# Kernel optimization log

Hardware: AMD Instinct MI355X
Metric: run time of the kernel (lower is better)

Reference implementation:

```python
import jax, jax.numpy as jnp
import numpy as np

N_NODES = 50000
N_EDGES = 800000
N_GRAPHS = 256
DROPOUT = 0.3


def _dropout(x, key, rate=DROPOUT):
    keep = 1.0 - rate
    mask = jax.random.bernoulli(key, keep, x.shape)
    return jnp.where(mask, x / keep, 0.0).astype(x.dtype)


def _gcn_conv(x, W, b, src, dst, num_nodes):
    # PyG GCNConv: symmetric norm with self-loops, edge_weight = 1.
    # deg over destination (col) including self-loop.
    deg = jnp.zeros((num_nodes,), x.dtype).at[dst].add(1.0) + 1.0
    dinv = jax.lax.rsqrt(deg)                       # [N]
    h = x @ W                                       # [N, F] GEMM first (F small)
    norm = dinv[src] * dinv[dst]                    # [E]
    msg = h[src] * norm[:, None]                    # [E, F] gather + scale
    agg = jnp.zeros_like(h).at[dst].add(msg)        # scatter-add
    agg = agg + h * (dinv * dinv)[:, None]          # self-loop contribution
    return agg + b


def setup_inputs() -> dict:
    key = jax.random.key(0)
    ks = jax.random.split(key, 8)
    d_in, d_h, d_out = 64, 64, 10
    s = lambda k, sh, fan: jax.random.normal(k, sh, jnp.float32) / np.sqrt(fan)
    return {
        "x": jax.random.normal(ks[0], (N_NODES, d_in), jnp.float32),
        "edge_index": jax.random.randint(ks[1], (2, N_EDGES), 0, N_NODES, jnp.int64),
        "batch": jnp.sort(jax.random.randint(ks[2], (N_NODES,), 0, N_GRAPHS, jnp.int64)),
        "W1": s(ks[3], (d_in, d_h), d_in), "b1": jnp.zeros((d_h,), jnp.float32),
        "W2": s(ks[4], (d_h, d_h), d_h),   "b2": jnp.zeros((d_h,), jnp.float32),
        "W3": s(ks[5], (d_h, d_h), d_h),   "b3": jnp.zeros((d_h,), jnp.float32),
        "Wl": s(ks[6], (d_h, d_out), d_h), "bl": jnp.zeros((d_out,), jnp.float32),
    }


def reference(x, edge_index, batch, W1, b1, W2, b2, W3, b3, Wl, bl):
    src, dst = edge_index[0], edge_index[1]
    dk = jax.random.split(jax.random.key(12345), 3)

    h = _gcn_conv(x, W1, b1, src, dst, N_NODES)
    h = _dropout(jax.nn.relu(h), dk[0])
    h = _gcn_conv(h, W2, b2, src, dst, N_NODES)
    h = _dropout(jax.nn.relu(h), dk[1])
    h = _gcn_conv(h, W3, b3, src, dst, N_NODES)

    # global mean pool over graphs
    sums = jax.ops.segment_sum(h, batch, num_segments=N_GRAPHS)          # [G, F]
    cnts = jax.ops.segment_sum(jnp.ones((h.shape[0],), h.dtype), batch,
                               num_segments=N_GRAPHS)                    # [G]
    pooled = sums / jnp.maximum(cnts, 1.0)[:, None]

    pooled = _dropout(pooled, dk[2])
    return pooled @ Wl + bl
```

## Files before the change

### kernel.cpp

```cpp
#include <hip/hip_runtime.h>

typedef unsigned int u32;
typedef unsigned short u16;
using bfrag  = __attribute__((ext_vector_type(8))) short;
using f32x4  = __attribute__((ext_vector_type(4))) float;

#define CHUNK 4096
#define KPT 16
#define NBUCK 128
#define BCAP 10496
#define CSRCAP (BCAP + 4096)

__host__ __device__ inline void tf2x32(u32 k0, u32 k1, u32 x0, u32 x1,
                                       u32* y0, u32* y1) {
    u32 ks2 = k0 ^ k1 ^ 0x1BD11BDAu;
#define TFR(r) { x0 += x1; x1 = (x1 << (r)) | (x1 >> (32 - (r))); x1 ^= x0; }
    x0 += k0; x1 += k1;
    TFR(13) TFR(15) TFR(26) TFR(6)
    x0 += k1;  x1 += ks2 + 1u;
    TFR(17) TFR(29) TFR(16) TFR(24)
    x0 += ks2; x1 += k0 + 2u;
    TFR(13) TFR(15) TFR(26) TFR(6)
    x0 += k0;  x1 += k1 + 3u;
    TFR(17) TFR(29) TFR(16) TFR(24)
    x0 += k1;  x1 += ks2 + 4u;
    TFR(13) TFR(15) TFR(26) TFR(6)
    x0 += ks2; x1 += k0 + 5u;
#undef TFR
    *y0 = x0; *y1 = x1;
}

__device__ inline float drop_scale(float v, u32 k0, u32 k1, u32 idx) {
    u32 y0, y1;
    tf2x32(k0, k1, 0u, idx, &y0, &y1);
    u32 bits = y0 ^ y1;
    float u = __uint_as_float((bits >> 9) | 0x3f800000u) - 1.0f;
    return (u < 0.7f) ? (v / 0.7f) : 0.0f;
}

__device__ inline u16 f2bf(float f) {
    u32 u = __float_as_uint(f);
    u32 r = (u + 0x7fffu + ((u >> 16) & 1u)) >> 16;
    return (u16)r;
}
__device__ inline float bf2f(u16 h) { return __uint_as_float(((u32)h) << 16); }

__device__ inline int idx_at(const void* p, long i, int is64) {
    return is64 ? (int)((const long long*)p)[i] : ((const int*)p)[i];
}

__global__ void k_init(const u32* p, int* flag, int* gCur1,
                       const float* __restrict__ W0, const float* __restrict__ W1,
                       const float* __restrict__ W2, u16* __restrict__ wsw,
                       float* __restrict__ sums, int ZN, u16* __restrict__ Hb, int N) {
    if (blockIdx.x == 0) {
        int tid = threadIdx.x;
        if (tid < NBUCK) gCur1[tid] = tid * BCAP;
        if (tid < 64) Hb[((long)N << 6) + tid] = 0;
        for (int i = tid; i < ZN; i += 256) sums[i] = 0.0f;
        if (tid == 0) {
            int all0 = 1;
            for (int i = 0; i < 64; ++i)
                if (p[2 * i + 1] != 0u) { all0 = 0; break; }
            *flag = all0;
        }
        return;
    }
    int t = (blockIdx.x - 1) * 256 + threadIdx.x;
    if (t >= 3 * 4096) return;
    int layer = t >> 12, r = t & 4095;
    int nt = r >> 10, ks = (r >> 9) & 1, lane = (r >> 3) & 63, j = r & 7;
    const float* W = (layer == 0) ? W0 : ((layer == 1) ? W1 : W2);
    int k = ks * 32 + (lane >> 4) * 8 + j;
    int n = nt * 16 + (lane & 15);
    wsw[t] = f2bf(W[k * 64 + n]);
}

__global__ __launch_bounds__(256) void k_binscat(
    const void* ei, int E, const int* flag,
    int* __restrict__ gCur1, u32* __restrict__ binned) {
    __shared__ u32 stage[CHUNK];
    __shared__ int cnt[NBUCK], offsx[NBUCK], cur[NBUCK], gbase[NBUCK], scn[NBUCK];
    int tid = threadIdx.x;
    long base = (long)blockIdx.x * CHUNK;
    int is64 = *flag;
    if (tid < NBUCK) { cnt[tid] = 0; cur[tid] = 0; }
    __syncthreads();
    u32 rec[KPT];
#pragma unroll
    for (int k = 0; k < KPT; ++k) {
        long e = base + k * 256 + tid;
        u32 r = 0xFFFFFFFFu;
        if (e < E) {
            int s = idx_at(ei, e, is64);
            int d = idx_at(ei, (long)E + e, is64);
            r = ((u32)d << 16) | (u32)s;
            atomicAdd(&cnt[d >> 9], 1);
        }
        rec[k] = r;
    }
    __syncthreads();
    if (tid < NBUCK) scn[tid] = cnt[tid];
    __syncthreads();
    for (int d = 1; d < NBUCK; d <<= 1) {
        int t2 = 0;
        if (tid < NBUCK && tid >= d) t2 = scn[tid - d];
        __syncthreads();
        if (tid < NBUCK) scn[tid] += t2;
        __syncthreads();
    }
    if (tid < NBUCK) offsx[tid] = scn[tid] - cnt[tid];
    __syncthreads();
#pragma unroll
    for (int k = 0; k < KPT; ++k) {
        u32 r = rec[k];
        if (r != 0xFFFFFFFFu) {
            int bk = r >> 25;
            int p = offsx[bk] + atomicAdd(&cur[bk], 1);
            stage[p] = r;
        }
    }
    __syncthreads();
    if (tid < NBUCK && cnt[tid] > 0)
        gbase[tid] = atomicAdd(&gCur1[tid], cnt[tid]);
    __syncthreads();
    int total = scn[NBUCK - 1];
    for (int i = tid; i < total; i += 256) {
        u32 r = stage[i];
        int bk = r >> 25;
        binned[gbase[bk] + (i - offsx[bk])] = r;
    }
}

__global__ __launch_bounds__(512) void k_csrfill(
    const u32* __restrict__ binned, const int* __restrict__ gCur1,
    int* __restrict__ offs, int* __restrict__ degi, float* __restrict__ dinv,
    u16* __restrict__ csr, int N) {
    __shared__ int lcnt[512];
    __shared__ int lcur[512];
    int b = blockIdx.x;
    int n0 = b << 9;
    int nn = N - n0; if (nn > 512) nn = 512;
    int tid = threadIdx.x;
    lcnt[tid] = 0;
    __syncthreads();
    int rbeg = b * BCAP, rend = gCur1[b];
    for (int i = rbeg + tid; i < rend; i += 512)
        atomicAdd(&lcnt[(int)(binned[i] >> 16) - n0], 1);
    __syncthreads();
    int v = lcnt[tid];
    int pv = (v + 7) & ~7;
    __syncthreads();
    lcnt[tid] = pv;
    __syncthreads();
    for (int d = 1; d < 512; d <<= 1) {
        int t2 = (tid >= d) ? lcnt[tid - d] : 0;
        __syncthreads();
        lcnt[tid] += t2;
        __syncthreads();
    }
    int pexcl = lcnt[tid] - pv;
    int o = b * CSRCAP + pexcl;
    if (tid < nn) {
        offs[n0 + tid] = o;
        degi[n0 + tid] = v;
        dinv[n0 + tid] = rsqrtf((float)v + 1.0f);
        lcur[tid] = o;
        for (int i = v; i < pv; ++i) csr[o + i] = (u16)N;
    }
    __syncthreads();
    for (int i = rbeg + tid; i < rend; i += 512) {
        u32 r = binned[i];
        int pos = atomicAdd(&lcur[(int)(r >> 16) - n0], 1);
        csr[pos] = (u16)(r & 0xFFFFu);
    }
}

__global__ __launch_bounds__(256) void k_gemm_mfma(
    const u16* __restrict__ Ab, const float* __restrict__ Af,
    const u16* __restrict__ Wsw, const float* __restrict__ dinv,
    u16* __restrict__ Hout, int N, int use_f32) {
    int wid = blockIdx.x * 4 + (threadIdx.x >> 6);
    int lane = threadIdx.x & 63;
    int row0 = wid * 16;
    if (row0 >= N) return;
    int rl = lane & 15, kg = lane >> 4;
    int arow = row0 + rl; if (arow >= N) arow = N - 1;
    bfrag a0, a1;
    if (use_f32) {
        const float* r = Af + (long)arow * 64 + kg * 8;
        float4 v0 = *(const float4*)(r);
        float4 v1 = *(const float4*)(r + 4);
        float4 v2 = *(const float4*)(r + 32);
        float4 v3 = *(const float4*)(r + 36);
        a0[0] = (short)f2bf(v0.x); a0[1] = (short)f2bf(v0.y);
        a0[2] = (short)f2bf(v0.z); a0[3] = (short)f2bf(v0.w);
        a0[4] = (short)f2bf(v1.x); a0[5] = (short)f2bf(v1.y);
        a0[6] = (short)f2bf(v1.z); a0[7] = (short)f2bf(v1.w);
        a1[0] = (short)f2bf(v2.x); a1[1] = (short)f2bf(v2.y);
        a1[2] = (short)f2bf(v2.z); a1[3] = (short)f2bf(v2.w);
        a1[4] = (short)f2bf(v3.x); a1[5] = (short)f2bf(v3.y);
        a1[6] = (short)f2bf(v3.z); a1[7] = (short)f2bf(v3.w);
    } else {
        a0 = *(const bfrag*)(Ab + (long)arow * 64 + kg * 8);
        a1 = *(const bfrag*)(Ab + (long)arow * 64 + 32 + kg * 8);
    }
    float d4[4];
#pragma unroll
    for (int i = 0; i < 4; ++i) {
        int row = row0 + kg * 4 + i;
        d4[i] = (row < N) ? dinv[row] : 0.0f;
    }
#pragma unroll
    for (int nt = 0; nt < 4; ++nt) {
        bfrag b0 = *(const bfrag*)(Wsw + ((nt * 2 + 0) * 64 + lane) * 8);
        bfrag b1 = *(const bfrag*)(Wsw + ((nt * 2 + 1) * 64 + lane) * 8);
        f32x4 acc = {0.0f, 0.0f, 0.0f, 0.0f};
        acc = __builtin_amdgcn_mfma_f32_16x16x32_bf16(a0, b0, acc, 0, 0, 0);
        acc = __builtin_amdgcn_mfma_f32_16x16x32_bf16(a1, b1, acc, 0, 0, 0);
        int col = nt * 16 + rl;
#pragma unroll
        for (int i = 0; i < 4; ++i) {
            int row = row0 + kg * 4 + i;
            if (row < N) Hout[(long)row * 64 + col] = f2bf(d4[i] * acc[i]);
        }
    }
}

__global__ __launch_bounds__(256) void k_agg(
    const u16* __restrict__ csr, const int* __restrict__ offs,
    const int* __restrict__ degi, const float* __restrict__ dinv,
    const u16* __restrict__ Hb, const float* __restrict__ b,
    u16* __restrict__ Gb, int N, int mode, u32 k0, u32 k1) {
    long t = (long)blockIdx.x * blockDim.x + threadIdx.x;
    int node = (int)(t >> 4);
    int q = (int)(t & 15);
    if (node >= N) return;
    int beg = offs[node];
    int deg = degi[node];
    int pv = (deg + 7) & ~7;
    float a0 = 0.0f, a1 = 0.0f, a2 = 0.0f, a3 = 0.0f;
    const u16* cp = csr + beg;
    ushort4 cA, cB;
    if (pv > 0) {
        cA = *(const ushort4*)cp;
        cB = *(const ushort4*)(cp + 4);
    }
    for (int g = 0; g < pv; g += 8) {
        ushort4 nA = *(const ushort4*)(cp + g + 8);
        ushort4 nB = *(const ushort4*)(cp + g + 12);
        u16 ids[8] = {cA.x, cA.y, cA.z, cA.w, cB.x, cB.y, cB.z, cB.w};
#pragma unroll
        for (int u = 0; u < 8; ++u) {
            uint2 d = *(const uint2*)(Hb + ((long)ids[u] << 6) + (q << 2));
            a0 += __uint_as_float(d.x << 16);
            a1 += __uint_as_float(d.x & 0xffff0000u);
            a2 += __uint_as_float(d.y << 16);
            a3 += __uint_as_float(d.y & 0xffff0000u);
        }
        cA = nA; cB = nB;
    }
    float di = dinv[node];
    uint2 hd = *(const uint2*)(Hb + ((long)node << 6) + (q << 2));
    float4 bv = *(const float4*)(b + (q << 2));
    float v0 = di * (a0 + __uint_as_float(hd.x << 16))         + bv.x;
    float v1 = di * (a1 + __uint_as_float(hd.x & 0xffff0000u)) + bv.y;
    float v2 = di * (a2 + __uint_as_float(hd.y << 16))         + bv.z;
    float v3 = di * (a3 + __uint_as_float(hd.y & 0xffff0000u)) + bv.w;
    u32 idx = ((u32)node << 6) + (q << 2);
    if (mode) {
        v0 = drop_scale(fmaxf(v0, 0.0f), k0, k1, idx + 0);
        v1 = drop_scale(fmaxf(v1, 0.0f), k0, k1, idx + 1);
        v2 = drop_scale(fmaxf(v2, 0.0f), k0, k1, idx + 2);
        v3 = drop_scale(fmaxf(v3, 0.0f), k0, k1, idx + 3);
    }
    ushort4 o; o.x = f2bf(v0); o.y = f2bf(v1); o.z = f2bf(v2); o.w = f2bf(v3);
    *(ushort4*)(Gb + idx) = o;
}

__global__ void k_poolsum(const u16* __restrict__ Gb, const void* batch,
                          const int* flag, int N,
                          float* __restrict__ sums, float* __restrict__ cnt) {
    int wave = (int)(((long)blockIdx.x * blockDim.x + threadIdx.x) >> 6);
    int f = threadIdx.x & 63;
    int n0 = wave * 8;
    if (n0 >= N) return;
    int nend = n0 + 8 < N ? n0 + 8 : N;
    int is64 = *flag;
    float acc = 0.0f; float cacc = 0.0f; int curg = -1;
    for (int n = n0; n < nend; ++n) {
        int g = idx_at(batch, n, is64);
        if (g != curg) {
            if (curg >= 0) {
                atomicAdd(&sums[curg * 64 + f], acc);
                if (f == 0) atomicAdd(&cnt[curg], cacc);
            }
            curg = g; acc = 0.0f; cacc = 0.0f;
        }
        acc += bf2f(Gb[(long)n * 64 + f]);
        cacc += 1.0f;
    }
    if (curg >= 0) {
        atomicAdd(&sums[curg * 64 + f], acc);
        if (f == 0) atomicAdd(&cnt[curg], cacc);
    }
}

__global__ void k_poolout(const float* __restrict__ sums, const float* __restrict__ cnt,
                          const float* __restrict__ Wl, const float* __restrict__ bl,
                          float* __restrict__ out, u32 k0, u32 k1, int O) {
    __shared__ float p_sh[64];
    int g = blockIdx.x;
    int t = threadIdx.x;
    float c = fmaxf(cnt[g], 1.0f);
    float pv = drop_scale(sums[g * 64 + t] / c, k0, k1, (u32)(g * 64 + t));
    p_sh[t] = pv;
    __syncthreads();
    if (t < O) {
        float acc = bl[t];
#pragma unroll 8
        for (int k = 0; k < 64; ++k) acc += p_sh[k] * Wl[k * O + t];
        out[g * O + t] = acc;
    }
}

extern "C" void kernel_launch(void* const* d_in, const int* in_sizes, int n_in,
                              void* d_out, int out_size, void* d_ws, size_t ws_size,
                              hipStream_t stream) {
    const float* x  = (const float*)d_in[0];
    const void*  ei = d_in[1];
    const void*  bt = d_in[2];
    const float* W[3] = {(const float*)d_in[3], (const float*)d_in[5], (const float*)d_in[7]};
    const float* b[3] = {(const float*)d_in[4], (const float*)d_in[6], (const float*)d_in[8]};
    const float* Wl = (const float*)d_in[9];
    const float* bl = (const float*)d_in[10];
    float* out = (float*)d_out;

    const int F = 64;
    int N  = in_sizes[0] / F;
    int E  = in_sizes[1] / 2;
    int NG = 256;
    int O  = in_sizes[9] / F;
    long NF = (long)N * F;
    int Np = ((N + 63) / 64) * 64;
    int NB = (N + 511) >> 9;

    auto align256 = [](char*& p) { p = (char*)(((size_t)p + 255) & ~(size_t)255); };
    char* wp = (char*)d_ws;
    align256(wp); float* dinv   = (float*)wp;  wp += (size_t)Np * 4;
    align256(wp); int*   degi   = (int*)wp;    wp += (size_t)Np * 4;
    align256(wp); int*   offs   = (int*)wp;    wp += (size_t)Np * 4;
    align256(wp); int*   flag   = (int*)wp;    wp += 256;
    align256(wp); int*   gCur1  = (int*)wp;    wp += NBUCK * 4;
    align256(wp); float* sums   = (float*)wp;  wp += (size_t)NG * F * 4;
    align256(wp); float* cnt    = (float*)wp;  wp += (size_t)NG * 4;
    align256(wp); u16*   wsw    = (u16*)wp;    wp += 3 * 4096 * 2;
    align256(wp); u32*   binned = (u32*)wp;    wp += (size_t)NBUCK * BCAP * 4;
    align256(wp); u16*   csr    = (u16*)wp;    wp += (size_t)NBUCK * CSRCAP * 2;
    align256(wp); u16*   Hb     = (u16*)wp;    wp += NF * 2 + 128;
    align256(wp); u16*   Gb     = (u16*)wp;    wp += NF * 2;

    u32 dk[3][2];
    for (u32 i = 0; i < 3; ++i) tf2x32(0u, 12345u, 0u, i, &dk[i][0], &dk[i][1]);

    int EB = (E + CHUNK - 1) / CHUNK;
    int ZN = NG * F + NG;

    k_init<<<49, 256, 0, stream>>>((const u32*)ei, flag, gCur1,
                                   W[0], W[1], W[2], wsw, sums, ZN, Hb, N);
    k_binscat<<<EB, 256, 0, stream>>>(ei, E, flag, gCur1, binned);
    k_csrfill<<<NB, 512, 0, stream>>>(binned, gCur1, offs, degi, dinv, csr, N);

    int gemmBlocks = ((N + 15) / 16 + 3) / 4;
    int aggBlocks = (int)(((long)N * 16 + 255) / 256);
    for (int l = 0; l < 3; ++l) {
        k_gemm_mfma<<<gemmBlocks, 256, 0, stream>>>(Gb, x, wsw + l * 4096, dinv,
                                                    Hb, N, (l == 0) ? 1 : 0);
        k_agg<<<aggBlocks, 256, 0, stream>>>(csr, offs, degi, dinv, Hb, b[l],
                                             Gb, N, (l < 2) ? 1 : 0,
                                             dk[l][0], dk[l][1]);
    }

    int pw = (N + 7) / 8;
    k_poolsum<<<(int)(((long)pw * 64 + 255) / 256), 256, 0, stream>>>(Gb, bt, flag, N, sums, cnt);
    k_poolout<<<NG, 64, 0, stream>>>(sums, cnt, Wl, bl, out, dk[2][0], dk[2][1], O);
}
```

Baseline: 137.7 us.

## Fuse next-layer GEMM into aggregation and simplify edge binning with fixed slots

Layers 1 and 2 now run one kernel that aggregates neighbours, applies bias, ReLU and dropout, stages the 16-node tile in shared memory, and multiplies by the next weight matrix with MFMA. This removes two GEMM launches and the round trip of the intermediate activation through global memory. Edge binning drops the per-block prefix scan in favour of fixed 72-slot shared buckets, with overflow going to a small list or to direct global atomics. The catch is that each aggregation block now also holds the GEMM work, and skewed buckets can push extra traffic onto global atomics.

```diff
diff --git a/kernel.cpp b/kernel.cpp
--- a/kernel.cpp
+++ b/kernel.cpp
@@ -8,6 +8,7 @@
 #define CHUNK 4096
 #define KPT 16
 #define NBUCK 128
+#define SCAP 72
 #define BCAP 10496
 #define CSRCAP (BCAP + 4096)
 
@@ -52,11 +53,15 @@
 __global__ void k_init(const u32* p, int* flag, int* gCur1,
                        const float* __restrict__ W0, const float* __restrict__ W1,
                        const float* __restrict__ W2, u16* __restrict__ wsw,
-                       float* __restrict__ sums, int ZN, u16* __restrict__ Hb, int N) {
+                       float* __restrict__ sums, int ZN,
+                       u16* __restrict__ HbA, u16* __restrict__ HbB, int N) {
     if (blockIdx.x == 0) {
         int tid = threadIdx.x;
         if (tid < NBUCK) gCur1[tid] = tid * BCAP;
-        if (tid < 64) Hb[((long)N << 6) + tid] = 0;
+        if (tid < 64) {
+            HbA[((long)N << 6) + tid] = 0;
+            HbB[((long)N << 6) + tid] = 0;
+        }
         for (int i = tid; i < ZN; i += 256) sums[i] = 0.0f;
         if (tid == 0) {
             int all0 = 1;
@@ -79,56 +84,51 @@
 __global__ __launch_bounds__(256) void k_binscat(
     const void* ei, int E, const int* flag,
     int* __restrict__ gCur1, u32* __restrict__ binned) {
-    __shared__ u32 stage[CHUNK];
-    __shared__ int cnt[NBUCK], offsx[NBUCK], cur[NBUCK], gbase[NBUCK], scn[NBUCK];
+    __shared__ u32 stage[NBUCK * SCAP];
+    __shared__ int cnt[NBUCK], gbase[NBUCK];
+    __shared__ u32 olist[256];
+    __shared__ int ocnt;
     int tid = threadIdx.x;
+    if (tid < NBUCK) cnt[tid] = 0;
+    if (tid == 0) ocnt = 0;
+    __syncthreads();
+    int is64 = *flag;
     long base = (long)blockIdx.x * CHUNK;
-    int is64 = *flag;
-    if (tid < NBUCK) { cnt[tid] = 0; cur[tid] = 0; }
-    __syncthreads();
-    u32 rec[KPT];
 #pragma unroll
     for (int k = 0; k < KPT; ++k) {
         long e = base + k * 256 + tid;
-        u32 r = 0xFFFFFFFFu;
         if (e < E) {
             int s = idx_at(ei, e, is64);
             int d = idx_at(ei, (long)E + e, is64);
-            r = ((u32)d << 16) | (u32)s;
-            atomicAdd(&cnt[d >> 9], 1);
-        }
-        rec[k] = r;
-    }
-    __syncthreads();
-    if (tid < NBUCK) scn[tid] = cnt[tid];
-    __syncthreads();
-    for (int d = 1; d < NBUCK; d <<= 1) {
-        int t2 = 0;
-        if (tid < NBUCK && tid >= d) t2 = scn[tid - d];
-        __syncthreads();
-        if (tid < NBUCK) scn[tid] += t2;
-        __syncthreads();
-    }
-    if (tid < NBUCK) offsx[tid] = scn[tid] - cnt[tid];
-    __syncthreads();
-#pragma unroll
-    for (int k = 0; k < KPT; ++k) {
-        u32 r = rec[k];
-        if (r != 0xFFFFFFFFu) {
-            int bk = r >> 25;
-            int p = offsx[bk] + atomicAdd(&cur[bk], 1);
-            stage[p] = r;
-        }
-    }
-    __syncthreads();
-    if (tid < NBUCK && cnt[tid] > 0)
-        gbase[tid] = atomicAdd(&gCur1[tid], cnt[tid]);
-    __syncthreads();
-    int total = scn[NBUCK - 1];
-    for (int i = tid; i < total; i += 256) {
-        u32 r = stage[i];
+            u32 r = ((u32)d << 16) | (u32)s;
+            int bk = d >> 9;
+            int pos = atomicAdd(&cnt[bk], 1);
+            if (pos < SCAP) stage[bk * SCAP + pos] = r;
+            else {
+                int op = atomicAdd(&ocnt, 1);
+                if (op < 256) olist[op] = r;
+                else { int pg = atomicAdd(&gCur1[bk], 1); binned[pg] = r; }
+            }
+        }
+    }
+    __syncthreads();
+    if (tid < NBUCK) {
+        int c = cnt[tid]; if (c > SCAP) c = SCAP;
+        cnt[tid] = c;
+        gbase[tid] = (c > 0) ? atomicAdd(&gCur1[tid], c) : 0;
+    }
+    __syncthreads();
+    int oc = ocnt; if (oc > 256) oc = 256;
+    for (int i = tid; i < oc; i += 256) {
+        u32 r = olist[i];
         int bk = r >> 25;
-        binned[gbase[bk] + (i - offsx[bk])] = r;
+        int pg = atomicAdd(&gCur1[bk], 1);
+        binned[pg] = r;
+    }
+    int wv = tid >> 6, lane = tid & 63;
+    for (int bk = wv * 32; bk < wv * 32 + 32; ++bk) {
+        int c = cnt[bk], gb = gbase[bk];
+        for (int i = lane; i < c; i += 64) binned[gb + i] = stage[bk * SCAP + i];
     }
 }
 
@@ -177,9 +177,8 @@
 }
 
 __global__ __launch_bounds__(256) void k_gemm_mfma(
-    const u16* __restrict__ Ab, const float* __restrict__ Af,
-    const u16* __restrict__ Wsw, const float* __restrict__ dinv,
-    u16* __restrict__ Hout, int N, int use_f32) {
+    const float* __restrict__ Af, const u16* __restrict__ Wsw,
+    const float* __restrict__ dinv, u16* __restrict__ Hout, int N) {
     int wid = blockIdx.x * 4 + (threadIdx.x >> 6);
     int lane = threadIdx.x & 63;
     int row0 = wid * 16;
@@ -187,7 +186,7 @@
     int rl = lane & 15, kg = lane >> 4;
     int arow = row0 + rl; if (arow >= N) arow = N - 1;
     bfrag a0, a1;
-    if (use_f32) {
+    {
         const float* r = Af + (long)arow * 64 + kg * 8;
         float4 v0 = *(const float4*)(r);
         float4 v1 = *(const float4*)(r + 4);
@@ -201,9 +200,6 @@
         a1[2] = (short)f2bf(v2.z); a1[3] = (short)f2bf(v2.w);
         a1[4] = (short)f2bf(v3.x); a1[5] = (short)f2bf(v3.y);
         a1[6] = (short)f2bf(v3.z); a1[7] = (short)f2bf(v3.w);
-    } else {
-        a0 = *(const bfrag*)(Ab + (long)arow * 64 + kg * 8);
-        a1 = *(const bfrag*)(Ab + (long)arow * 64 + 32 + kg * 8);
     }
     float d4[4];
 #pragma unroll
@@ -227,11 +223,86 @@
     }
 }
 
-__global__ __launch_bounds__(256) void k_agg(
+__global__ __launch_bounds__(256) void k_aggf(
     const u16* __restrict__ csr, const int* __restrict__ offs,
     const int* __restrict__ degi, const float* __restrict__ dinv,
     const u16* __restrict__ Hb, const float* __restrict__ b,
-    u16* __restrict__ Gb, int N, int mode, u32 k0, u32 k1) {
+    const u16* __restrict__ Wsw, u16* __restrict__ Hout,
+    int N, u32 k0, u32 k1) {
+    __shared__ u32 Gs[16][36];
+    __shared__ float dsh[16];
+    int tid = threadIdx.x;
+    int nl = tid >> 4;
+    int q  = tid & 15;
+    int node = blockIdx.x * 16 + nl;
+    u32 gx = 0, gy = 0;
+    if (node < N) {
+        int beg = offs[node];
+        int deg = degi[node];
+        int pv = (deg + 7) & ~7;
+        float a0 = 0.0f, a1 = 0.0f, a2 = 0.0f, a3 = 0.0f;
+        const u16* cp = csr + beg;
+        ushort4 cA, cB;
+        if (pv > 0) { cA = *(const ushort4*)cp; cB = *(const ushort4*)(cp + 4); }
+        for (int g = 0; g < pv; g += 8) {
+            ushort4 nA = *(const ushort4*)(cp + g + 8);
+            ushort4 nB = *(const ushort4*)(cp + g + 12);
+            u16 ids[8] = {cA.x, cA.y, cA.z, cA.w, cB.x, cB.y, cB.z, cB.w};
+#pragma unroll
+            for (int u = 0; u < 8; ++u) {
+                uint2 d = *(const uint2*)(Hb + ((long)ids[u] << 6) + (q << 2));
+                a0 += __uint_as_float(d.x << 16);
+                a1 += __uint_as_float(d.x & 0xffff0000u);
+                a2 += __uint_as_float(d.y << 16);
+                a3 += __uint_as_float(d.y & 0xffff0000u);
+            }
+            cA = nA; cB = nB;
+        }
+        float di = dinv[node];
+        if (q == 0) dsh[nl] = di;
+        uint2 hd = *(const uint2*)(Hb + ((long)node << 6) + (q << 2));
+        float4 bv = *(const float4*)(b + (q << 2));
+        float v0 = di * (a0 + __uint_as_float(hd.x << 16))         + bv.x;
+        float v1 = di * (a1 + __uint_as_float(hd.x & 0xffff0000u)) + bv.y;
+        float v2 = di * (a2 + __uint_as_float(hd.y << 16))         + bv.z;
+        float v3 = di * (a3 + __uint_as_float(hd.y & 0xffff0000u)) + bv.w;
+        u32 idx = ((u32)node << 6) + (q << 2);
+        v0 = drop_scale(fmaxf(v0, 0.0f), k0, k1, idx + 0);
+        v1 = drop_scale(fmaxf(v1, 0.0f), k0, k1, idx + 1);
+        v2 = drop_scale(fmaxf(v2, 0.0f), k0, k1, idx + 2);
+        v3 = drop_scale(fmaxf(v3, 0.0f), k0, k1, idx + 3);
+        gx = (u32)f2bf(v0) | ((u32)f2bf(v1) << 16);
+        gy = (u32)f2bf(v2) | ((u32)f2bf(v3) << 16);
+    } else if (q == 0) {
+        dsh[nl] = 0.0f;
+    }
+    Gs[nl][q * 2]     = gx;
+    Gs[nl][q * 2 + 1] = gy;
+    __syncthreads();
+    int wv = tid >> 6;
+    int lane = tid & 63;
+    int rl = lane & 15, kg = lane >> 4;
+    bfrag a0f = *(const bfrag*)&Gs[rl][kg * 4];
+    bfrag a1f = *(const bfrag*)&Gs[rl][16 + kg * 4];
+    bfrag b0 = *(const bfrag*)(Wsw + ((wv * 2 + 0) * 64 + lane) * 8);
+    bfrag b1 = *(const bfrag*)(Wsw + ((wv * 2 + 1) * 64 + lane) * 8);
+    f32x4 acc = {0.0f, 0.0f, 0.0f, 0.0f};
+    acc = __builtin_amdgcn_mfma_f32_16x16x32_bf16(a0f, b0, acc, 0, 0, 0);
+    acc = __builtin_amdgcn_mfma_f32_16x16x32_bf16(a1f, b1, acc, 0, 0, 0);
+    int col = wv * 16 + rl;
+    int row0 = blockIdx.x * 16;
+#pragma unroll
+    for (int i = 0; i < 4; ++i) {
+        int row = row0 + kg * 4 + i;
+        if (row < N) Hout[(long)row * 64 + col] = f2bf(dsh[kg * 4 + i] * acc[i]);
+    }
+}
+
+__global__ __launch_bounds__(256) void k_agg3(
+    const u16* __restrict__ csr, const int* __restrict__ offs,
+    const int* __restrict__ degi, const float* __restrict__ dinv,
+    const u16* __restrict__ Hb, const float* __restrict__ b,
+    u16* __restrict__ Gb, int N) {
     long t = (long)blockIdx.x * blockDim.x + threadIdx.x;
     int node = (int)(t >> 4);
     int q = (int)(t & 15);
@@ -242,10 +313,7 @@
     float a0 = 0.0f, a1 = 0.0f, a2 = 0.0f, a3 = 0.0f;
     const u16* cp = csr + beg;
     ushort4 cA, cB;
-    if (pv > 0) {
-        cA = *(const ushort4*)cp;
-        cB = *(const ushort4*)(cp + 4);
-    }
+    if (pv > 0) { cA = *(const ushort4*)cp; cB = *(const ushort4*)(cp + 4); }
     for (int g = 0; g < pv; g += 8) {
         ushort4 nA = *(const ushort4*)(cp + g + 8);
         ushort4 nB = *(const ushort4*)(cp + g + 12);
@@ -268,12 +336,6 @@
     float v2 = di * (a2 + __uint_as_float(hd.y << 16))         + bv.z;
     float v3 = di * (a3 + __uint_as_float(hd.y & 0xffff0000u)) + bv.w;
     u32 idx = ((u32)node << 6) + (q << 2);
-    if (mode) {
-        v0 = drop_scale(fmaxf(v0, 0.0f), k0, k1, idx + 0);
-        v1 = drop_scale(fmaxf(v1, 0.0f), k0, k1, idx + 1);
-        v2 = drop_scale(fmaxf(v2, 0.0f), k0, k1, idx + 2);
-        v3 = drop_scale(fmaxf(v3, 0.0f), k0, k1, idx + 3);
-    }
     ushort4 o; o.x = f2bf(v0); o.y = f2bf(v1); o.z = f2bf(v2); o.w = f2bf(v3);
     *(ushort4*)(Gb + idx) = o;
 }
@@ -357,8 +419,8 @@
     align256(wp); u16*   wsw    = (u16*)wp;    wp += 3 * 4096 * 2;
     align256(wp); u32*   binned = (u32*)wp;    wp += (size_t)NBUCK * BCAP * 4;
     align256(wp); u16*   csr    = (u16*)wp;    wp += (size_t)NBUCK * CSRCAP * 2;
-    align256(wp); u16*   Hb     = (u16*)wp;    wp += NF * 2 + 128;
-    align256(wp); u16*   Gb     = (u16*)wp;    wp += NF * 2;
+    align256(wp); u16*   HbA    = (u16*)wp;    wp += NF * 2 + 128;
+    align256(wp); u16*   HbB    = (u16*)wp;    wp += NF * 2 + 128;
 
     u32 dk[3][2];
     for (u32 i = 0; i < 3; ++i) tf2x32(0u, 12345u, 0u, i, &dk[i][0], &dk[i][1]);
@@ -367,21 +429,22 @@
     int ZN = NG * F + NG;
 
     k_init<<<49, 256, 0, stream>>>((const u32*)ei, flag, gCur1,
-                                   W[0], W[1], W[2], wsw, sums, ZN, Hb, N);
+                                   W[0], W[1], W[2], wsw, sums, ZN, HbA, HbB, N);
     k_binscat<<<EB, 256, 0, stream>>>(ei, E, flag, gCur1, binned);
     k_csrfill<<<NB, 512, 0, stream>>>(binned, gCur1, offs, degi, dinv, csr, N);
 
     int gemmBlocks = ((N + 15) / 16 + 3) / 4;
-    int aggBlocks = (int)(((long)N * 16 + 255) / 256);
-    for (int l = 0; l < 3; ++l) {
-        k_gemm_mfma<<<gemmBlocks, 256, 0, stream>>>(Gb, x, wsw + l * 4096, dinv,
-                                                    Hb, N, (l == 0) ? 1 : 0);
-        k_agg<<<aggBlocks, 256, 0, stream>>>(csr, offs, degi, dinv, Hb, b[l],
-                                             Gb, N, (l < 2) ? 1 : 0,
-                                             dk[l][0], dk[l][1]);
-    }
+    int nodeBlocks = (N + 15) / 16;
+    int aggBlocks  = (int)(((long)N * 16 + 255) / 256);
+
+    k_gemm_mfma<<<gemmBlocks, 256, 0, stream>>>(x, wsw, dinv, HbA, N);
+    k_aggf<<<nodeBlocks, 256, 0, stream>>>(csr, offs, degi, dinv, HbA, b[0],
+                                           wsw + 4096, HbB, N, dk[0][0], dk[0][1]);
+    k_aggf<<<nodeBlocks, 256, 0, stream>>>(csr, offs, degi, dinv, HbB, b[1],
+                                           wsw + 8192, HbA, N, dk[1][0], dk[1][1]);
+    k_agg3<<<aggBlocks, 256, 0, stream>>>(csr, offs, degi, dinv, HbA, b[2], HbB, N);
 
     int pw = (N + 7) / 8;
-    k_poolsum<<<(int)(((long)pw * 64 + 255) / 256), 256, 0, stream>>>(Gb, bt, flag, N, sums, cnt);
+    k_poolsum<<<(int)(((long)pw * 64 + 255) / 256), 256, 0, stream>>>(HbB, bt, flag, N, sums, cnt);
     k_poolout<<<NG, 64, 0, stream>>>(sums, cnt, Wl, bl, out, dk[2][0], dk[2][1], O);
 }
```

New measurement: 125.7 us. 1.1x faster.
